# Optimization experiments

Hardware: AMD Instinct MI355X
Metric: run time of the kernel (lower is better)

## Reference

```python
import jax, jax.numpy as jnp
import numpy as np

B, U, N, D, O = 64, 8, 2048, 512, 512  # batch, units, neurons, input_dim, output_dim
RES_CONN, IN_CONN, BIAS_P = 0.2, 0.2, 0.5


def setup_inputs() -> dict:
    key = jax.random.key(0)
    ks = jax.random.split(key, 10)
    # Recurrent weights: normal * sparse mask, normalized by ~spectral radius
    Wd = jax.random.normal(ks[0], (U, N, N), dtype=jnp.float32)
    Wmask = (jax.random.uniform(ks[1], (U, N, N)) < RES_CONN).astype(jnp.float32)
    W = Wd * Wmask / jnp.sqrt(RES_CONN * N)  # approx unit spectral radius
    # Input weights: fixed_bernoulli -> {0,1} sparse matrix
    Win = (jax.random.uniform(ks[2], (U, D, N)) < IN_CONN).astype(jnp.float32)
    bias = (jax.random.uniform(ks[3], (U, 1, N)) < BIAS_P).astype(jnp.float32)
    Wout = jax.random.normal(ks[4], (U, N, O), dtype=jnp.float32)
    sr = jax.random.uniform(ks[5], (U, 1, 1), dtype=jnp.float32)
    adaptive_lr = jax.random.uniform(ks[6], (U, D, 1), dtype=jnp.float32)
    temperature = jnp.ones((1,), dtype=jnp.float32)
    X = jax.random.normal(ks[7], (B, U, D), dtype=jnp.float32)
    state = jax.random.normal(ks[8], (B, U, N), dtype=jnp.float32)
    return {"X": X, "state": state, "W": W, "Win": Win, "bias": bias,
            "Wout": Wout, "sr": sr, "adaptive_lr": adaptive_lr,
            "temperature": temperature}


def reference(X, state, W, Win, bias, Wout, sr, adaptive_lr, temperature):
    # X: [B,U,D], state: [B,U,N]
    x = X[:, :, None, :]       # [B,U,1,D]
    s = state[:, :, None, :]   # [B,U,1,N]
    # adaptive learning rate: softmax over units
    logits = jnp.einsum('buid,udk->buik', x, adaptive_lr) / temperature  # [B,U,1,1]
    lr = jax.nn.softmax(logits, axis=1)
    # _sparse_mm_subhead == masked matmul (W's zeros contribute nothing)
    feed = jnp.einsum('bud,udn->bun', X, Win)[:, :, None, :]           # [B,U,1,N]
    echo = jnp.einsum('bun,unm->bum', state, W * sr)[:, :, None, :] + bias
    new_state = (1.0 - lr) * s + lr * jnp.tanh(feed + echo)            # [B,U,1,N]
    output = jnp.einsum('buin,uno->buio', new_state, Wout)             # [B,U,1,O]
    return new_state.squeeze(2), output.squeeze(2)
```

## Files before the change

### kernel.cpp

```cpp
#include <hip/hip_runtime.h>

#define B_ 64
#define U_ 8
#define N_ 2048
#define D_ 512
#define O_ 512
#define NS_ELEMS ((long)B_ * U_ * N_)
#define OUT_ELEMS ((long)B_ * U_ * O_)

typedef __attribute__((ext_vector_type(8))) short short8;
typedef __attribute__((ext_vector_type(8))) float float8;
typedef __attribute__((ext_vector_type(4))) float float4v;
typedef __attribute__((ext_vector_type(4))) unsigned short ushort4v;
typedef __attribute__((ext_vector_type(16))) float floatx16;

__device__ __forceinline__ float bf2f(unsigned short b) {
    unsigned int u = ((unsigned int)b) << 16;
    float f; __builtin_memcpy(&f, &u, 4); return f;
}
__device__ __forceinline__ unsigned short f2bf(float f) {
    unsigned int u; __builtin_memcpy(&u, &f, 4);
    u += 0x7FFFu + ((u >> 16) & 1u);
    return (unsigned short)(u >> 16);
}
__device__ __forceinline__ bool is_bf(const void* temp) {
    return ((const unsigned short*)temp)[0] == 0x3F80u;
}
__device__ __forceinline__ float ldg1(const void* p, long i, bool bf) {
    return bf ? bf2f(((const unsigned short*)p)[i]) : ((const float*)p)[i];
}
__device__ __forceinline__ short8 ld8(const void* p, long i, bool bf) {
    if (bf) return *(const short8*)((const unsigned short*)p + i);
    float8 v = *(const float8*)((const float*)p + i);
    short8 r;
#pragma unroll
    for (int e = 0; e < 8; ++e) r[e] = (short)f2bf(v[e]);
    return r;
}
__device__ __forceinline__ short8 ld8s(const void* p, long i, bool bf, float s) {
    short8 r;
    if (bf) {
        short8 v = *(const short8*)((const unsigned short*)p + i);
#pragma unroll
        for (int e = 0; e < 8; ++e) r[e] = (short)f2bf(bf2f((unsigned short)v[e]) * s);
    } else {
        float8 v = *(const float8*)((const float*)p + i);
#pragma unroll
        for (int e = 0; e < 8; ++e) r[e] = (short)f2bf(v[e] * s);
    }
    return r;
}
__device__ __forceinline__ void stg1(void* p, long i, bool bf, float v) {
    if (bf) ((unsigned short*)p)[i] = f2bf(v); else ((float*)p)[i] = v;
}
__device__ __forceinline__ int swz(int row, int kbyte) {
    return row * 128 + (kbyte ^ ((row & 7) << 4));
}

__device__ __forceinline__ void gl_lds16(const void* g, void* l) {
    __builtin_amdgcn_global_load_lds(
        (const __attribute__((address_space(1))) unsigned int*)g,
        (__attribute__((address_space(3))) unsigned int*)l, 16, 0, 0);
}
#define WAITV(n) asm volatile("s_waitcnt vmcnt(" #n ")" ::: "memory")

template<bool BF, int NCH>
__device__ __forceinline__ void gemm_stream(
        const char* __restrict__ Apan, long arow_b,
        const char* __restrict__ Bpan, long brow_b,
        char* __restrict__ As,
        char* __restrict__ Bs,
        floatx16& acc, int t) {
    const int w = t >> 6, l = t & 63;
    const int mrow = (w >> 1) * 32 + (l & 31);
    const int ncol = (w & 1) * 32 + (l & 31);
    const int BCH = BF ? 8192 : 16384;
    const int a_r = w * 16 + (l >> 3);
    const long a_g = 16 * ((l & 7) ^ (l >> 3));

#define ISSUE(ck)                                                                   \
    {   char* Ad = As + ((ck) % 3) * 8192 + w * 2048;                               \
        const char* Ag0 = Apan + (long)(ck) * 128;                                  \
        gl_lds16(Ag0 + (long)a_r * arow_b + a_g, Ad);                               \
        gl_lds16(Ag0 + (long)(a_r + 8) * arow_b + a_g, Ad + 1024);                  \
        char* Bd = Bs + ((ck) % 3) * BCH;                                           \
        if (BF) {                                                                   \
            const char* Bg0 = Bpan +                                                \
                (long)((ck) * 64 + w * 16 + (l >> 3)) * brow_b + (l & 7) * 16;      \
            gl_lds16(Bg0, Bd + w * 2048);                                           \
            gl_lds16(Bg0 + 8 * brow_b, Bd + w * 2048 + 1024);                       \
        } else {                                                                    \
            const char* Bg0 = Bpan +                                                \
                (long)((ck) * 64 + w * 16 + (l >> 4)) * brow_b + (l & 15) * 16;     \
            gl_lds16(Bg0, Bd + w * 4096);                                           \
            gl_lds16(Bg0 + 4 * brow_b, Bd + w * 4096 + 1024);                       \
            gl_lds16(Bg0 + 8 * brow_b, Bd + w * 4096 + 2048);                       \
            gl_lds16(Bg0 + 12 * brow_b, Bd + w * 4096 + 3072);                      \
        } }

    ISSUE(0);
    ISSUE(1);
#pragma unroll
    for (int ck = 0; ck < NCH; ++ck) {
        if (ck + 2 < NCH) ISSUE(ck + 2);
        __builtin_amdgcn_sched_barrier(0);
        const int rem = NCH - 1 - ck;
        if (BF) { if (rem >= 2) WAITV(8); else if (rem == 1) WAITV(4); else WAITV(0); }
        else    { if (rem >= 2) WAITV(12); else if (rem == 1) WAITV(6); else WAITV(0); }
        __builtin_amdgcn_s_barrier();
        __builtin_amdgcn_sched_barrier(0);
        const char* Ac = As + (ck % 3) * 8192;
        const char* Bc = Bs + (ck % 3) * BCH;
#pragma unroll
        for (int ks = 0; ks < 4; ++ks) {
            int g = 2 * ks + (l >> 5);
            short8 a = *(const short8*)(Ac + swz(mrow, g * 16));
            short8 bfr;
            if (BF) {
#pragma unroll
                for (int e = 0; e < 8; ++e)
                    bfr[e] = *(const short*)(Bc + (g * 8 + e) * 128 + ncol * 2);
            } else {
#pragma unroll
                for (int e = 0; e < 8; ++e)
                    bfr[e] = (short)f2bf(*(const float*)(Bc + (g * 8 + e) * 256 + ncol * 4));
            }
            acc = __builtin_amdgcn_mfma_f32_32x32x16_bf16(a, bfr, acc, 0, 0, 0);
        }
        __builtin_amdgcn_sched_barrier(0);
        __builtin_amdgcn_s_barrier();
    }
#undef ISSUE
}

__global__ __launch_bounds__(256) void k0_pack(
        const void* __restrict__ state, const void* __restrict__ X,
        const void* __restrict__ sr, const void* __restrict__ temp,
        unsigned short* __restrict__ stC, unsigned short* __restrict__ xC) {
    const bool bf = is_bf(temp);
    const long i = ((long)blockIdx.x * 256 + threadIdx.x) * 4;
    ushort4v o;
    if (i < NS_ELEMS) {
        const int u = (int)(i >> 17), b = (int)((i >> 11) & 63), k = (int)(i & 2047);
        const float srv = ldg1(sr, u, bf);
#pragma unroll
        for (int e = 0; e < 4; ++e)
            o[e] = f2bf(ldg1(state, (long)(b * 8 + u) * 2048 + k + e, bf) * srv);
        *(ushort4v*)(stC + i) = o;
    } else {
        const long j = i - NS_ELEMS;
        const int u = (int)(j >> 15), b = (int)((j >> 9) & 63), k = (int)(j & 511);
#pragma unroll
        for (int e = 0; e < 4; ++e)
            o[e] = f2bf(ldg1(X, (long)(b * 8 + u) * 512 + k + e, bf));
        *(ushort4v*)(xC + j) = o;
    }
}

__global__ __launch_bounds__(512) void k1_lr(
        const void* __restrict__ X, const void* __restrict__ alr,
        const void* __restrict__ temp, float* __restrict__ lrbuf) {
    const bool bf = is_bf(temp);
    const int b = blockIdx.x;
    const int t = threadIdx.x;
    const int u = t >> 6, ln = t & 63;
    float s = 0.f;
#pragma unroll
    for (int e = 0; e < 8; ++e) {
        int d = ln * 8 + e;
        s += ldg1(X, (long)(b * 8 + u) * 512 + d, bf) * ldg1(alr, u * 512 + d, bf);
    }
#pragma unroll
    for (int off = 1; off < 64; off <<= 1) s += __shfl_xor(s, off);
    __shared__ float lg[U_];
    const float T = ldg1(temp, 0, bf);
    if (ln == 0) lg[u] = s / T;
    __syncthreads();
    if (t < U_) {
        float m = lg[0];
#pragma unroll
        for (int i = 1; i < U_; ++i) m = fmaxf(m, lg[i]);
        float den = 0.f;
#pragma unroll
        for (int i = 0; i < U_; ++i) den += expf(lg[i] - m);
        lrbuf[b * U_ + t] = expf(lg[t] - m) / den;
    }
}

template<bool BF>
__device__ __forceinline__ void k2s_body(
        const unsigned short* stC, const unsigned short* xC,
        const void* W, const void* Win, unsigned short* slabs,
        char* As, char* Bs, int bid, int t) {
    const int seg = bid >> 8;
    const int u   = (bid >> 5) & 7;
    const int n0  = (bid & 31) * 64;
    const int w = t >> 6, l = t & 63;
    const long esz = BF ? 2 : 4;
    floatx16 acc;
#pragma unroll
    for (int i = 0; i < 16; ++i) acc[i] = 0.f;

    const char* stP = (const char*)stC + (long)u * 262144;
    const char* Wp  = (const char*)W + ((long)u * N_ * N_ + n0) * esz;

    if (seg == 0) {
        gemm_stream<BF, 8>((const char*)xC + (long)u * 65536, 1024,
                           (const char*)Win + ((long)u * D_ * N_ + n0) * esz, N_ * esz,
                           As, Bs, acc, t);
        gemm_stream<BF, 8>(stP, 4096, Wp, N_ * esz, As, Bs, acc, t);
    } else if (seg == 1) {
        gemm_stream<BF, 12>(stP + 1024, 4096, Wp + (long)512 * N_ * esz, N_ * esz,
                            As, Bs, acc, t);
    } else {
        gemm_stream<BF, 12>(stP + 2560, 4096, Wp + (long)1280 * N_ * esz, N_ * esz,
                            As, Bs, acc, t);
    }
    unsigned short* slab = slabs + (long)seg * NS_ELEMS;
    const int n = n0 + (w & 1) * 32 + (l & 31);
    const int rowbase = (w >> 1) * 32 + 4 * (l >> 5);
#pragma unroll
    for (int r = 0; r < 16; ++r) {
        int b = rowbase + (r & 3) + 8 * (r >> 2);
        slab[(long)b * (U_ * N_) + u * N_ + n] = f2bf(acc[r]);
    }
}

__global__ __launch_bounds__(256) void k2_stream(
        const unsigned short* __restrict__ stC, const unsigned short* __restrict__ xC,
        const void* __restrict__ W, const void* __restrict__ Win,
        const void* __restrict__ temp, unsigned short* __restrict__ slabs) {
    __shared__ alignas(16) char As[3 * 8192];
    __shared__ alignas(16) char Bs[3 * 16384];
    const int bid = (blockIdx.x % 8) * 96 + blockIdx.x / 8;
    if (is_bf(temp))
        k2s_body<true >(stC, xC, W, Win, slabs, As, Bs, bid, threadIdx.x);
    else
        k2s_body<false>(stC, xC, W, Win, slabs, As, Bs, bid, threadIdx.x);
}

__global__ void k2b_mix(const unsigned short* __restrict__ slabs,
                        const void* __restrict__ state,
                        const void* __restrict__ bias, const void* __restrict__ temp,
                        const float* __restrict__ lrbuf, void* __restrict__ ns,
                        unsigned short* __restrict__ nsC) {
    const bool bf = is_bf(temp);
    const long i = ((long)blockIdx.x * 256 + threadIdx.x) * 4;
    const int b = (int)(i >> 14);
    const int un = (int)(i & 16383);
    const int u = un >> 11, n = un & 2047;
    float4v s;
    {
        ushort4v v0 = *(const ushort4v*)(slabs + i);
        ushort4v v1 = *(const ushort4v*)(slabs + NS_ELEMS + i);
        ushort4v v2 = *(const ushort4v*)(slabs + 2 * NS_ELEMS + i);
#pragma unroll
        for (int e = 0; e < 4; ++e) s[e] = bf2f(v0[e]) + bf2f(v1[e]) + bf2f(v2[e]);
    }
    const float lr = lrbuf[b * U_ + u];
    ushort4v oc;
#pragma unroll
    for (int e = 0; e < 4; ++e) {
        float st = ldg1(state, i + e, bf);
        float bv = ldg1(bias, u * N_ + n + e, bf);
        float v = (1.f - lr) * st + lr * tanhf(s[e] + bv);
        stg1(ns, i + e, bf, v);
        oc[e] = f2bf(v);
    }
    *(ushort4v*)(nsC + ((long)u * 64 + b) * 2048 + n) = oc;
}

template<bool BF>
__device__ __forceinline__ void k3s_body(
        const unsigned short* nsC, const void* Wout, unsigned short* part,
        char* As, char* Bs, int bid, int t) {
    const int kc = bid >> 6;
    const int u  = (bid >> 3) & 7;
    const int ot = bid & 7;
    const int o0 = ot * 64;
    const int w = t >> 6, l = t & 63;
    const long esz = BF ? 2 : 4;
    floatx16 acc;
#pragma unroll
    for (int i = 0; i < 16; ++i) acc[i] = 0.f;
    gemm_stream<BF, 4>((const char*)nsC + (long)u * 262144 + (long)kc * 512, 4096,
                       (const char*)Wout + ((long)u * N_ * O_ + (long)kc * 256 * O_ + o0) * esz,
                       O_ * esz, As, Bs, acc, t);
    unsigned short* slab = part + (((kc * 8 + u) * 8 + ot) << 12);
    const int oo = (w & 1) * 32 + (l & 31);
    const int rowbase = (w >> 1) * 32 + 4 * (l >> 5);
#pragma unroll
    for (int r = 0; r < 16; ++r) {
        int b = rowbase + (r & 3) + 8 * (r >> 2);
        slab[b * 64 + oo] = f2bf(acc[r]);
    }
}

__global__ __launch_bounds__(256) void k3_stream(
        const unsigned short* __restrict__ nsC, const void* __restrict__ Wout,
        const void* __restrict__ temp, unsigned short* __restrict__ part) {
    __shared__ alignas(16) char As[3 * 8192];
    __shared__ alignas(16) char Bs[3 * 16384];
    const int bid = (blockIdx.x % 8) * 64 + blockIdx.x / 8;
    if (is_bf(temp))
        k3s_body<true >(nsC, Wout, part, As, Bs, bid, threadIdx.x);
    else
        k3s_body<false>(nsC, Wout, part, As, Bs, bid, threadIdx.x);
}

__global__ void k3_reduce(const unsigned short* __restrict__ part,
                          const void* __restrict__ temp,
                          void* __restrict__ outfull) {
    const bool bf = is_bf(temp);
    int i = blockIdx.x * 256 + threadIdx.x;
    int b = i >> 12;
    int u = (i >> 9) & 7;
    int o = i & 511;
    int ot = o >> 6, oo = o & 63;
    float s = 0.f;
#pragma unroll
    for (int kc = 0; kc < 8; ++kc)
        s += bf2f(part[(((kc * 8 + u) * 8 + ot) << 12) + b * 64 + oo]);
    stg1(outfull, NS_ELEMS + i, bf, s);
}

__global__ __launch_bounds__(256) void k2_state(
        const void* __restrict__ X, const void* __restrict__ state,
        const void* __restrict__ W, const void* __restrict__ Win,
        const void* __restrict__ bias, const void* __restrict__ sr,
        const void* __restrict__ temp, const float* __restrict__ lrbuf,
        void* __restrict__ ns) {
    const bool bf = is_bf(temp);
    const int u  = blockIdx.x >> 5;
    const int n0 = (blockIdx.x & 31) * 64;
    const int t = threadIdx.x;
    const int w = t >> 6, l = t & 63;
    __shared__ alignas(16) char As[8192];
    __shared__ alignas(16) char Bs[8192];
    const float srv = ldg1(sr, u, bf);
    floatx16 acc;
#pragma unroll
    for (int i = 0; i < 16; ++i) acc[i] = 0.f;
    for (int ck = 0; ck < 40; ++ck) {
        const bool feed = ck < 8;
        const void* Ag; long aoff; int lda; float ascale;
        const void* Bg; long boff;
        if (feed) {
            Ag = X;   aoff = (long)u * D_ + ck * 64;          lda = U_ * D_; ascale = 1.f;
            Bg = Win; boff = (long)u * D_ * N_ + (long)(ck * 64) * N_ + n0;
        } else {
            Ag = state; aoff = (long)u * N_ + (ck - 8) * 64;  lda = U_ * N_; ascale = srv;
            Bg = W;     boff = (long)u * N_ * N_ + (long)((ck - 8) * 64) * N_ + n0;
        }
        __syncthreads();
#pragma unroll
        for (int j = 0; j < 2; ++j) {
            int idx = j * 256 + t;
            int row = idx >> 3, cch = idx & 7;
            short8 v = ld8s(Ag, aoff + (long)row * lda + cch * 8, bf, ascale);
            *(short8*)(As + swz(row, cch * 16)) = v;
        }
#pragma unroll
        for (int j = 0; j < 2; ++j) {
            int k = t & 63;
            int c = (t >> 6) + 4 * j;
            short8 v = ld8(Bg, boff + (long)k * N_ + c * 8, bf);
#pragma unroll
            for (int e = 0; e < 8; ++e) {
                int n = c * 8 + e;
                *(unsigned short*)(Bs + swz(n, 2 * k)) = (unsigned short)v[e];
            }
        }
        __syncthreads();
        const int mrow = (w >> 1) * 32 + (l & 31);
        const int ncol = (w & 1) * 32 + (l & 31);
#pragma unroll
        for (int ks = 0; ks < 4; ++ks) {
            int g = 2 * ks + (l >> 5);
            short8 a = *(const short8*)(As + swz(mrow, g * 16));
            short8 b = *(const short8*)(Bs + swz(ncol, g * 16));
            acc = __builtin_amdgcn_mfma_f32_32x32x16_bf16(a, b, acc, 0, 0, 0);
        }
    }
    const int n = n0 + (w & 1) * 32 + (l & 31);
    const int rowbase = (w >> 1) * 32 + 4 * (l >> 5);
    const float biasv = ldg1(bias, u * N_ + n, bf);
#pragma unroll
    for (int r = 0; r < 16; ++r) {
        int b = rowbase + (r & 3) + 8 * (r >> 2);
        float lr = lrbuf[b * U_ + u];
        float st = ldg1(state, (long)b * U_ * N_ + u * N_ + n, bf);
        float v = (1.f - lr) * st + lr * tanhf(acc[r] + biasv);
        stg1(ns, (long)b * U_ * N_ + u * N_ + n, bf, v);
    }
}

__global__ __launch_bounds__(256) void k3_mono(
        const void* __restrict__ ns, const void* __restrict__ Wout,
        const void* __restrict__ temp, void* __restrict__ outfull) {
    const bool bf = is_bf(temp);
    const int u  = (blockIdx.x >> 3) & 7;
    const int ot = blockIdx.x & 7;
    const int o0 = ot * 64;
    const int t = threadIdx.x;
    const int w = t >> 6, l = t & 63;
    __shared__ alignas(16) char As[8192];
    __shared__ alignas(16) char Bs[8192];
    floatx16 acc;
#pragma unroll
    for (int i = 0; i < 16; ++i) acc[i] = 0.f;
    for (int ck = 0; ck < 32; ++ck) {
        const long ka = (long)(ck * 64);
        __syncthreads();
#pragma unroll
        for (int j = 0; j < 2; ++j) {
            int idx = j * 256 + t;
            int row = idx >> 3, cch = idx & 7;
            short8 v = ld8(ns, (long)row * (U_ * N_) + u * N_ + ka + cch * 8, bf);
            *(short8*)(As + swz(row, cch * 16)) = v;
        }
#pragma unroll
        for (int j = 0; j < 2; ++j) {
            int k = t & 63;
            int c = (t >> 6) + 4 * j;
            short8 v = ld8(Wout, (long)u * N_ * O_ + (ka + k) * O_ + o0 + c * 8, bf);
#pragma unroll
            for (int e = 0; e < 8; ++e) {
                int n = c * 8 + e;
                *(unsigned short*)(Bs + swz(n, 2 * k)) = (unsigned short)v[e];
            }
        }
        __syncthreads();
        const int mrow = (w >> 1) * 32 + (l & 31);
        const int ncol = (w & 1) * 32 + (l & 31);
#pragma unroll
        for (int ks = 0; ks < 4; ++ks) {
            int g = 2 * ks + (l >> 5);
            short8 a = *(const short8*)(As + swz(mrow, g * 16));
            short8 b = *(const short8*)(Bs + swz(ncol, g * 16));
            acc = __builtin_amdgcn_mfma_f32_32x32x16_bf16(a, b, acc, 0, 0, 0);
        }
    }
    const int oo = (w & 1) * 32 + (l & 31);
    const int rowbase = (w >> 1) * 32 + 4 * (l >> 5);
#pragma unroll
    for (int r = 0; r < 16; ++r) {
        int b = rowbase + (r & 3) + 8 * (r >> 2);
        stg1(outfull, NS_ELEMS + (long)b * U_ * O_ + u * O_ + o0 + oo, bf, acc[r]);
    }
}

extern "C" void kernel_launch(void* const* d_in, const int* in_sizes, int n_in,
                              void* d_out, int out_size, void* d_ws, size_t ws_size,
                              hipStream_t stream) {
    const void* X     = d_in[0];
    const void* state = d_in[1];
    const void* W     = d_in[2];
    const void* Win   = d_in[3];
    const void* bias  = d_in[4];
    const void* Wout  = d_in[5];
    const void* sr    = d_in[6];
    const void* alr   = d_in[7];
    const void* temp  = d_in[8];

    char* base = (char*)d_ws;
    float* lrbuf        = (float*)base;
    unsigned short* stC = (unsigned short*)(base + 4096);
    unsigned short* xC  = (unsigned short*)(base + 4096 + (2u << 20));
    unsigned short* nsC = (unsigned short*)(base + 4096 + (2u << 20) + (512u << 10));
    unsigned short* slabs = (unsigned short*)(base + (8u << 20));
    const size_t need = (8u << 20) + 3 * (size_t)NS_ELEMS * 2;

    k1_lr<<<B_, 512, 0, stream>>>(X, alr, temp, lrbuf);

    if (ws_size >= need) {
        k0_pack  <<<1280, 256, 0, stream>>>(state, X, sr, temp, stC, xC);
        k2_stream<<<768, 256, 0, stream>>>(stC, xC, W, Win, temp, slabs);
        k2b_mix  <<<NS_ELEMS / 1024, 256, 0, stream>>>(slabs, state, bias, temp, lrbuf, d_out, nsC);
        k3_stream<<<512, 256, 0, stream>>>(nsC, Wout, temp, slabs);
        k3_reduce<<<OUT_ELEMS / 256, 256, 0, stream>>>(slabs, temp, d_out);
    } else {
        k2_state<<<256, 256, 0, stream>>>(X, state, W, Win, bias, sr, temp, lrbuf, d_out);
        k3_mono <<<64, 256, 0, stream>>>(d_out, Wout, temp, d_out);
    }
}
```

Measured before the change: 66.99 us.

## Widen GEMM tiles to 64x128, double-buffer, rebalance split-K, fuse pack and lr

The streaming GEMM helper now computes a 64x128 tile with two MFMA accumulators per wave, so each A fragment load feeds two MFMAs. It also switches from triple to double buffering of the LDS stages. The recurrent GEMM is re-split into four K segments over 128-wide N tiles, and the mix kernel sums four partial slabs instead of three. The output GEMM uses 128-wide O tiles with a matching reduce layout. The pack and learning-rate kernels are merged into one launch to save a launch. The trade-offs are fewer blocks, higher LDS use per block (lower occupancy), a shallower prefetch pipeline, and an extra slab of workspace traffic.

```diff
diff --git a/kernel.cpp b/kernel.cpp
--- a/kernel.cpp
+++ b/kernel.cpp
@@ -65,178 +65,194 @@
 #define WAITV(n) asm volatile("s_waitcnt vmcnt(" #n ")" ::: "memory")
 
 template<bool BF, int NCH>
-__device__ __forceinline__ void gemm_stream(
+__device__ __forceinline__ void gemm_wide(
         const char* __restrict__ Apan, long arow_b,
         const char* __restrict__ Bpan, long brow_b,
         char* __restrict__ As,
         char* __restrict__ Bs,
-        floatx16& acc, int t) {
+        floatx16& acc0, floatx16& acc1, int t) {
     const int w = t >> 6, l = t & 63;
     const int mrow = (w >> 1) * 32 + (l & 31);
-    const int ncol = (w & 1) * 32 + (l & 31);
-    const int BCH = BF ? 8192 : 16384;
+    const int nc0 = (w & 1) * 64 + (l & 31);
+    const int BCH = BF ? 16384 : 32768;
     const int a_r = w * 16 + (l >> 3);
     const long a_g = 16 * ((l & 7) ^ (l >> 3));
 
-#define ISSUE(ck)                                                                   \
-    {   char* Ad = As + ((ck) % 3) * 8192 + w * 2048;                               \
+#define ISSUE2(ck)                                                                  \
+    {   char* Ad = As + ((ck) & 1) * 8192 + w * 2048;                               \
         const char* Ag0 = Apan + (long)(ck) * 128;                                  \
         gl_lds16(Ag0 + (long)a_r * arow_b + a_g, Ad);                               \
         gl_lds16(Ag0 + (long)(a_r + 8) * arow_b + a_g, Ad + 1024);                  \
-        char* Bd = Bs + ((ck) % 3) * BCH;                                           \
+        char* Bd = Bs + ((ck) & 1) * BCH;                                           \
         if (BF) {                                                                   \
-            const char* Bg0 = Bpan +                                                \
-                (long)((ck) * 64 + w * 16 + (l >> 3)) * brow_b + (l & 7) * 16;      \
-            gl_lds16(Bg0, Bd + w * 2048);                                           \
-            gl_lds16(Bg0 + 8 * brow_b, Bd + w * 2048 + 1024);                       \
+            _Pragma("unroll")                                                       \
+            for (int i = 0; i < 4; ++i) {                                           \
+                int kr = (ck) * 64 + w * 16 + i * 4 + (l >> 4);                     \
+                gl_lds16(Bpan + (long)kr * brow_b + (l & 15) * 16,                  \
+                         Bd + (w * 16 + i * 4) * 256);                              \
+            }                                                                       \
         } else {                                                                    \
-            const char* Bg0 = Bpan +                                                \
-                (long)((ck) * 64 + w * 16 + (l >> 4)) * brow_b + (l & 15) * 16;     \
-            gl_lds16(Bg0, Bd + w * 4096);                                           \
-            gl_lds16(Bg0 + 4 * brow_b, Bd + w * 4096 + 1024);                       \
-            gl_lds16(Bg0 + 8 * brow_b, Bd + w * 4096 + 2048);                       \
-            gl_lds16(Bg0 + 12 * brow_b, Bd + w * 4096 + 3072);                      \
+            _Pragma("unroll")                                                       \
+            for (int i = 0; i < 8; ++i) {                                           \
+                int kr = (ck) * 64 + w * 16 + i * 2 + (l >> 5);                     \
+                gl_lds16(Bpan + (long)kr * brow_b + (l & 31) * 16,                  \
+                         Bd + (w * 16 + i * 2) * 512);                              \
+            }                                                                       \
         } }
 
-    ISSUE(0);
-    ISSUE(1);
+    ISSUE2(0);
 #pragma unroll
     for (int ck = 0; ck < NCH; ++ck) {
-        if (ck + 2 < NCH) ISSUE(ck + 2);
+        if (ck + 1 < NCH) ISSUE2(ck + 1);
         __builtin_amdgcn_sched_barrier(0);
-        const int rem = NCH - 1 - ck;
-        if (BF) { if (rem >= 2) WAITV(8); else if (rem == 1) WAITV(4); else WAITV(0); }
-        else    { if (rem >= 2) WAITV(12); else if (rem == 1) WAITV(6); else WAITV(0); }
+        if (ck + 1 < NCH) { if (BF) { WAITV(6); } else { WAITV(10); } }
+        else { WAITV(0); }
         __builtin_amdgcn_s_barrier();
         __builtin_amdgcn_sched_barrier(0);
-        const char* Ac = As + (ck % 3) * 8192;
-        const char* Bc = Bs + (ck % 3) * BCH;
+        const char* Ac = As + (ck & 1) * 8192;
+        const char* Bc = Bs + (ck & 1) * BCH;
 #pragma unroll
         for (int ks = 0; ks < 4; ++ks) {
             int g = 2 * ks + (l >> 5);
             short8 a = *(const short8*)(Ac + swz(mrow, g * 16));
-            short8 bfr;
+            short8 b0, b1;
             if (BF) {
 #pragma unroll
-                for (int e = 0; e < 8; ++e)
-                    bfr[e] = *(const short*)(Bc + (g * 8 + e) * 128 + ncol * 2);
+                for (int e = 0; e < 8; ++e) {
+                    b0[e] = *(const short*)(Bc + (g * 8 + e) * 256 + nc0 * 2);
+                    b1[e] = *(const short*)(Bc + (g * 8 + e) * 256 + (nc0 + 32) * 2);
+                }
             } else {
 #pragma unroll
-                for (int e = 0; e < 8; ++e)
-                    bfr[e] = (short)f2bf(*(const float*)(Bc + (g * 8 + e) * 256 + ncol * 4));
+                for (int e = 0; e < 8; ++e) {
+                    b0[e] = (short)f2bf(*(const float*)(Bc + (g * 8 + e) * 512 + nc0 * 4));
+                    b1[e] = (short)f2bf(*(const float*)(Bc + (g * 8 + e) * 512 + (nc0 + 32) * 4));
+                }
             }
-            acc = __builtin_amdgcn_mfma_f32_32x32x16_bf16(a, bfr, acc, 0, 0, 0);
+            acc0 = __builtin_amdgcn_mfma_f32_32x32x16_bf16(a, b0, acc0, 0, 0, 0);
+            acc1 = __builtin_amdgcn_mfma_f32_32x32x16_bf16(a, b1, acc1, 0, 0, 0);
         }
         __builtin_amdgcn_sched_barrier(0);
         __builtin_amdgcn_s_barrier();
     }
-#undef ISSUE
-}
-
-__global__ __launch_bounds__(256) void k0_pack(
+#undef ISSUE2
+}
+
+__global__ __launch_bounds__(256) void k01(
         const void* __restrict__ state, const void* __restrict__ X,
-        const void* __restrict__ sr, const void* __restrict__ temp,
-        unsigned short* __restrict__ stC, unsigned short* __restrict__ xC) {
+        const void* __restrict__ sr, const void* __restrict__ alr,
+        const void* __restrict__ temp,
+        unsigned short* __restrict__ stC, unsigned short* __restrict__ xC,
+        float* __restrict__ lrbuf) {
     const bool bf = is_bf(temp);
-    const long i = ((long)blockIdx.x * 256 + threadIdx.x) * 4;
-    ushort4v o;
-    if (i < NS_ELEMS) {
-        const int u = (int)(i >> 17), b = (int)((i >> 11) & 63), k = (int)(i & 2047);
-        const float srv = ldg1(sr, u, bf);
-#pragma unroll
-        for (int e = 0; e < 4; ++e)
-            o[e] = f2bf(ldg1(state, (long)(b * 8 + u) * 2048 + k + e, bf) * srv);
-        *(ushort4v*)(stC + i) = o;
+    const int bid = blockIdx.x;
+    const int t = threadIdx.x;
+    __shared__ float lg[U_];
+    if (bid < 1280) {
+        const long i = ((long)bid * 256 + t) * 4;
+        ushort4v o;
+        if (i < NS_ELEMS) {
+            const int u = (int)(i >> 17);
+            const float srv = ldg1(sr, u, bf);
+#pragma unroll
+            for (int e = 0; e < 4; ++e) {
+                const long j = i + e;
+                const int b = (int)((j >> 11) & 63), k = (int)(j & 2047);
+                o[e] = f2bf(ldg1(state, (long)(b * 8 + u) * 2048 + k, bf) * srv);
+            }
+            *(ushort4v*)(stC + i) = o;
+        } else {
+            const long j0 = i - NS_ELEMS;
+            const int u = (int)(j0 >> 15);
+#pragma unroll
+            for (int e = 0; e < 4; ++e) {
+                const long j = j0 + e;
+                const int b = (int)((j >> 9) & 63), k = (int)(j & 511);
+                o[e] = f2bf(ldg1(X, (long)(b * 8 + u) * 512 + k, bf));
+            }
+            *(ushort4v*)(xC + j0) = o;
+        }
     } else {
-        const long j = i - NS_ELEMS;
-        const int u = (int)(j >> 15), b = (int)((j >> 9) & 63), k = (int)(j & 511);
-#pragma unroll
-        for (int e = 0; e < 4; ++e)
-            o[e] = f2bf(ldg1(X, (long)(b * 8 + u) * 512 + k + e, bf));
-        *(ushort4v*)(xC + j) = o;
-    }
-}
-
-__global__ __launch_bounds__(512) void k1_lr(
-        const void* __restrict__ X, const void* __restrict__ alr,
-        const void* __restrict__ temp, float* __restrict__ lrbuf) {
-    const bool bf = is_bf(temp);
-    const int b = blockIdx.x;
-    const int t = threadIdx.x;
-    const int u = t >> 6, ln = t & 63;
-    float s = 0.f;
-#pragma unroll
-    for (int e = 0; e < 8; ++e) {
-        int d = ln * 8 + e;
-        s += ldg1(X, (long)(b * 8 + u) * 512 + d, bf) * ldg1(alr, u * 512 + d, bf);
-    }
-#pragma unroll
-    for (int off = 1; off < 64; off <<= 1) s += __shfl_xor(s, off);
-    __shared__ float lg[U_];
-    const float T = ldg1(temp, 0, bf);
-    if (ln == 0) lg[u] = s / T;
-    __syncthreads();
-    if (t < U_) {
-        float m = lg[0];
-#pragma unroll
-        for (int i = 1; i < U_; ++i) m = fmaxf(m, lg[i]);
-        float den = 0.f;
-#pragma unroll
-        for (int i = 0; i < U_; ++i) den += expf(lg[i] - m);
-        lrbuf[b * U_ + t] = expf(lg[t] - m) / den;
+        const int b = bid - 1280;
+        const int u = t >> 5, ln = t & 31;
+        float s = 0.f;
+#pragma unroll
+        for (int j = 0; j < 16; ++j) {
+            int d = ln * 16 + j;
+            s += ldg1(X, (long)(b * 8 + u) * 512 + d, bf) * ldg1(alr, u * 512 + d, bf);
+        }
+#pragma unroll
+        for (int off = 1; off < 32; off <<= 1) s += __shfl_xor(s, off);
+        const float T = ldg1(temp, 0, bf);
+        if (ln == 0) lg[u] = s / T;
+        __syncthreads();
+        if (t < U_) {
+            float m = lg[0];
+#pragma unroll
+            for (int i = 1; i < U_; ++i) m = fmaxf(m, lg[i]);
+            float den = 0.f;
+#pragma unroll
+            for (int i = 0; i < U_; ++i) den += expf(lg[i] - m);
+            lrbuf[b * U_ + t] = expf(lg[t] - m) / den;
+        }
     }
 }
 
 template<bool BF>
-__device__ __forceinline__ void k2s_body(
+__device__ __forceinline__ void k2w_body(
         const unsigned short* stC, const unsigned short* xC,
         const void* W, const void* Win, unsigned short* slabs,
         char* As, char* Bs, int bid, int t) {
-    const int seg = bid >> 8;
-    const int u   = (bid >> 5) & 7;
-    const int n0  = (bid & 31) * 64;
+    const int seg = bid >> 7;
+    const int u   = (bid >> 4) & 7;
+    const int nb  = bid & 15;
+    const int n0  = nb * 128;
     const int w = t >> 6, l = t & 63;
     const long esz = BF ? 2 : 4;
-    floatx16 acc;
-#pragma unroll
-    for (int i = 0; i < 16; ++i) acc[i] = 0.f;
+    floatx16 acc0, acc1;
+#pragma unroll
+    for (int i = 0; i < 16; ++i) { acc0[i] = 0.f; acc1[i] = 0.f; }
 
     const char* stP = (const char*)stC + (long)u * 262144;
     const char* Wp  = (const char*)W + ((long)u * N_ * N_ + n0) * esz;
 
     if (seg == 0) {
-        gemm_stream<BF, 8>((const char*)xC + (long)u * 65536, 1024,
-                           (const char*)Win + ((long)u * D_ * N_ + n0) * esz, N_ * esz,
-                           As, Bs, acc, t);
-        gemm_stream<BF, 8>(stP, 4096, Wp, N_ * esz, As, Bs, acc, t);
+        gemm_wide<BF, 8>((const char*)xC + (long)u * 65536, 1024,
+                         (const char*)Win + ((long)u * D_ * N_ + n0) * esz, N_ * esz,
+                         As, Bs, acc0, acc1, t);
+        gemm_wide<BF, 2>(stP, 4096, Wp, N_ * esz, As, Bs, acc0, acc1, t);
     } else if (seg == 1) {
-        gemm_stream<BF, 12>(stP + 1024, 4096, Wp + (long)512 * N_ * esz, N_ * esz,
-                            As, Bs, acc, t);
+        gemm_wide<BF, 10>(stP + 256, 4096, Wp + (long)128 * N_ * esz, N_ * esz,
+                          As, Bs, acc0, acc1, t);
+    } else if (seg == 2) {
+        gemm_wide<BF, 10>(stP + 1536, 4096, Wp + (long)768 * N_ * esz, N_ * esz,
+                          As, Bs, acc0, acc1, t);
     } else {
-        gemm_stream<BF, 12>(stP + 2560, 4096, Wp + (long)1280 * N_ * esz, N_ * esz,
-                            As, Bs, acc, t);
+        gemm_wide<BF, 10>(stP + 2816, 4096, Wp + (long)1408 * N_ * esz, N_ * esz,
+                          As, Bs, acc0, acc1, t);
     }
     unsigned short* slab = slabs + (long)seg * NS_ELEMS;
-    const int n = n0 + (w & 1) * 32 + (l & 31);
+    const int n = n0 + (w & 1) * 64 + (l & 31);
     const int rowbase = (w >> 1) * 32 + 4 * (l >> 5);
 #pragma unroll
     for (int r = 0; r < 16; ++r) {
         int b = rowbase + (r & 3) + 8 * (r >> 2);
-        slab[(long)b * (U_ * N_) + u * N_ + n] = f2bf(acc[r]);
-    }
-}
-
-__global__ __launch_bounds__(256) void k2_stream(
+        slab[(long)b * (U_ * N_) + u * N_ + n] = f2bf(acc0[r]);
+        slab[(long)b * (U_ * N_) + u * N_ + n + 32] = f2bf(acc1[r]);
+    }
+}
+
+__global__ __launch_bounds__(256) void k2_wide(
         const unsigned short* __restrict__ stC, const unsigned short* __restrict__ xC,
         const void* __restrict__ W, const void* __restrict__ Win,
         const void* __restrict__ temp, unsigned short* __restrict__ slabs) {
-    __shared__ alignas(16) char As[3 * 8192];
-    __shared__ alignas(16) char Bs[3 * 16384];
-    const int bid = (blockIdx.x % 8) * 96 + blockIdx.x / 8;
+    __shared__ alignas(16) char As[2 * 8192];
+    __shared__ alignas(16) char Bs[2 * 32768];
+    const int bid = (blockIdx.x % 8) * 64 + blockIdx.x / 8;
     if (is_bf(temp))
-        k2s_body<true >(stC, xC, W, Win, slabs, As, Bs, bid, threadIdx.x);
+        k2w_body<true >(stC, xC, W, Win, slabs, As, Bs, bid, threadIdx.x);
     else
-        k2s_body<false>(stC, xC, W, Win, slabs, As, Bs, bid, threadIdx.x);
+        k2w_body<false>(stC, xC, W, Win, slabs, As, Bs, bid, threadIdx.x);
 }
 
 __global__ void k2b_mix(const unsigned short* __restrict__ slabs,
@@ -254,8 +270,10 @@
         ushort4v v0 = *(const ushort4v*)(slabs + i);
         ushort4v v1 = *(const ushort4v*)(slabs + NS_ELEMS + i);
         ushort4v v2 = *(const ushort4v*)(slabs + 2 * NS_ELEMS + i);
-#pragma unroll
-        for (int e = 0; e < 4; ++e) s[e] = bf2f(v0[e]) + bf2f(v1[e]) + bf2f(v2[e]);
+        ushort4v v3 = *(const ushort4v*)(slabs + 3 * NS_ELEMS + i);
+#pragma unroll
+        for (int e = 0; e < 4; ++e)
+            s[e] = (bf2f(v0[e]) + bf2f(v1[e])) + (bf2f(v2[e]) + bf2f(v3[e]));
     }
     const float lr = lrbuf[b * U_ + u];
     ushort4v oc;
@@ -271,41 +289,42 @@
 }
 
 template<bool BF>
-__device__ __forceinline__ void k3s_body(
+__device__ __forceinline__ void k3w_body(
         const unsigned short* nsC, const void* Wout, unsigned short* part,
         char* As, char* Bs, int bid, int t) {
-    const int kc = bid >> 6;
-    const int u  = (bid >> 3) & 7;
-    const int ot = bid & 7;
-    const int o0 = ot * 64;
+    const int kc = bid >> 5;
+    const int u  = (bid >> 2) & 7;
+    const int ot = bid & 3;
+    const int o0 = ot * 128;
     const int w = t >> 6, l = t & 63;
     const long esz = BF ? 2 : 4;
-    floatx16 acc;
-#pragma unroll
-    for (int i = 0; i < 16; ++i) acc[i] = 0.f;
-    gemm_stream<BF, 4>((const char*)nsC + (long)u * 262144 + (long)kc * 512, 4096,
-                       (const char*)Wout + ((long)u * N_ * O_ + (long)kc * 256 * O_ + o0) * esz,
-                       O_ * esz, As, Bs, acc, t);
-    unsigned short* slab = part + (((kc * 8 + u) * 8 + ot) << 12);
-    const int oo = (w & 1) * 32 + (l & 31);
+    floatx16 acc0, acc1;
+#pragma unroll
+    for (int i = 0; i < 16; ++i) { acc0[i] = 0.f; acc1[i] = 0.f; }
+    gemm_wide<BF, 4>((const char*)nsC + (long)u * 262144 + (long)kc * 512, 4096,
+                     (const char*)Wout + ((long)u * N_ * O_ + (long)kc * 256 * O_ + o0) * esz,
+                     O_ * esz, As, Bs, acc0, acc1, t);
+    unsigned short* slab = part + (long)((kc * 8 + u) * 4 + ot) * 8192;
+    const int oo = (w & 1) * 64 + (l & 31);
     const int rowbase = (w >> 1) * 32 + 4 * (l >> 5);
 #pragma unroll
     for (int r = 0; r < 16; ++r) {
         int b = rowbase + (r & 3) + 8 * (r >> 2);
-        slab[b * 64 + oo] = f2bf(acc[r]);
-    }
-}
-
-__global__ __launch_bounds__(256) void k3_stream(
+        slab[b * 128 + oo] = f2bf(acc0[r]);
+        slab[b * 128 + oo + 32] = f2bf(acc1[r]);
+    }
+}
+
+__global__ __launch_bounds__(256) void k3_wide(
         const unsigned short* __restrict__ nsC, const void* __restrict__ Wout,
         const void* __restrict__ temp, unsigned short* __restrict__ part) {
-    __shared__ alignas(16) char As[3 * 8192];
-    __shared__ alignas(16) char Bs[3 * 16384];
-    const int bid = (blockIdx.x % 8) * 64 + blockIdx.x / 8;
+    __shared__ alignas(16) char As[2 * 8192];
+    __shared__ alignas(16) char Bs[2 * 32768];
+    const int bid = (blockIdx.x % 8) * 32 + blockIdx.x / 8;
     if (is_bf(temp))
-        k3s_body<true >(nsC, Wout, part, As, Bs, bid, threadIdx.x);
+        k3w_body<true >(nsC, Wout, part, As, Bs, bid, threadIdx.x);
     else
-        k3s_body<false>(nsC, Wout, part, As, Bs, bid, threadIdx.x);
+        k3w_body<false>(nsC, Wout, part, As, Bs, bid, threadIdx.x);
 }
 
 __global__ void k3_reduce(const unsigned short* __restrict__ part,
@@ -316,11 +335,11 @@
     int b = i >> 12;
     int u = (i >> 9) & 7;
     int o = i & 511;
-    int ot = o >> 6, oo = o & 63;
+    int ot = o >> 7, oo = o & 127;
     float s = 0.f;
 #pragma unroll
     for (int kc = 0; kc < 8; ++kc)
-        s += bf2f(part[(((kc * 8 + u) * 8 + ot) << 12) + b * 64 + oo]);
+        s += bf2f(part[(long)((kc * 8 + u) * 4 + ot) * 8192 + b * 128 + oo]);
     stg1(outfull, NS_ELEMS + i, bf, s);
 }
 
@@ -469,18 +488,18 @@
     unsigned short* xC  = (unsigned short*)(base + 4096 + (2u << 20));
     unsigned short* nsC = (unsigned short*)(base + 4096 + (2u << 20) + (512u << 10));
     unsigned short* slabs = (unsigned short*)(base + (8u << 20));
-    const size_t need = (8u << 20) + 3 * (size_t)NS_ELEMS * 2;
-
-    k1_lr<<<B_, 512, 0, stream>>>(X, alr, temp, lrbuf);
+    const size_t need = (8u << 20) + 4 * (size_t)NS_ELEMS * 2;
 
     if (ws_size >= need) {
-        k0_pack  <<<1280, 256, 0, stream>>>(state, X, sr, temp, stC, xC);
-        k2_stream<<<768, 256, 0, stream>>>(stC, xC, W, Win, temp, slabs);
+        k01      <<<1344, 256, 0, stream>>>(state, X, sr, alr, temp, stC, xC, lrbuf);
+        k2_wide  <<<512, 256, 0, stream>>>(stC, xC, W, Win, temp, slabs);
         k2b_mix  <<<NS_ELEMS / 1024, 256, 0, stream>>>(slabs, state, bias, temp, lrbuf, d_out, nsC);
-        k3_stream<<<512, 256, 0, stream>>>(nsC, Wout, temp, slabs);
+        k3_wide  <<<256, 256, 0, stream>>>(nsC, Wout, temp, slabs);
         k3_reduce<<<OUT_ELEMS / 256, 256, 0, stream>>>(slabs, temp, d_out);
     } else {
-        k2_state<<<256, 256, 0, stream>>>(X, state, W, Win, bias, sr, temp, lrbuf, d_out);
-        k3_mono <<<64, 256, 0, stream>>>(d_out, Wout, temp, d_out);
-    }
-}
+        k01      <<<1344, 256, 0, stream>>>(state, X, sr, alr, temp,
+                                            (unsigned short*)base, (unsigned short*)base, lrbuf);
+        k2_state <<<256, 256, 0, stream>>>(X, state, W, Win, bias, sr, temp, lrbuf, d_out);
+        k3_mono  <<<64, 256, 0, stream>>>(d_out, Wout, temp, d_out);
+    }
+}
```

New measurement: 59.48 us. -11.2%, faster.
